# Performance work log

Hardware: AMD Instinct MI355X
Metric: run time of the kernel (lower is better)

The kernel has to match this reference:

```python
import jax, jax.numpy as jnp
import numpy as np
import math

B, S, E, H, V, VOCAB = 32, 512, 1024, 8, 36, 32000
PAD = 32  # padding_idx in nn.Embedding


def setup_inputs() -> dict:
    key = jax.random.key(0)
    ks = jax.random.split(key, 10)
    tokens = jax.random.randint(ks[0], (B, S), 0, VOCAB, dtype=jnp.int32)
    emb = jax.random.normal(ks[1], (VOCAB + 1, E), jnp.float32) * 0.02
    emb = emb.at[PAD].set(0.0)  # padding_idx row is zero
    Wq = jax.random.normal(ks[2], (H, E, E), jnp.float32) * 0.02
    bq = jax.random.normal(ks[3], (H, E), jnp.float32) * 0.02
    Wk = jax.random.normal(ks[4], (H, E, E), jnp.float32) * 0.02
    bk = jax.random.normal(ks[5], (H, E), jnp.float32) * 0.02
    Wv = jax.random.normal(ks[6], (H, E, V), jnp.float32) * 0.02
    bv = jax.random.normal(ks[7], (H, V), jnp.float32) * 0.02
    fc_w = jax.random.normal(ks[8], (2, S * H * V), jnp.float32) * 0.02
    fc_b = jax.random.normal(ks[9], (2,), jnp.float32) * 0.02
    return {"tokens": tokens, "emb": emb, "Wq": Wq, "bq": bq, "Wk": Wk,
            "bk": bk, "Wv": Wv, "bv": bv, "fc_w": fc_w, "fc_b": fc_b}


def reference(tokens, emb, Wq, bq, Wk, bk, Wv, bv, fc_w, fc_b):
    x = emb[tokens]  # [B,S,E]
    # 8 independent ReLU-gated attention heads, batched over head dim h
    q = jax.nn.relu(jnp.einsum('bse,hef->hbsf', x, Wq) + bq[:, None, None, :])  # [H,B,S,E]
    k = jax.nn.relu(jnp.einsum('bse,hef->hbsf', x, Wk) + bk[:, None, None, :])  # [H,B,S,E]
    v = jax.nn.relu(jnp.einsum('bse,hev->hbsv', x, Wv) + bv[:, None, None, :])  # [H,B,S,V]
    scores = jnp.einsum('hbsf,hbtf->hbst', q, k) / math.sqrt(E)  # [H,B,S,S]
    attn = jax.nn.softmax(scores, axis=-1)
    out = jnp.einsum('hbst,hbtv->hbsv', attn, v)  # [H,B,S,V]
    # concat heads on last dim -> [B,S,H*V] -> flatten [B, S*H*V]
    feat = jnp.transpose(out, (1, 2, 0, 3)).reshape(B, S * H * V)
    logits = feat @ fc_w.T + fc_b  # [B,2]
    score = jax.nn.sigmoid(logits)
    pred = jax.nn.log_softmax(score, axis=1)
    return pred, score
```

## Files before the change

### kernel.cpp

```cpp
#include <hip/hip_runtime.h>
#include <cstdint>

typedef unsigned short u16;
typedef unsigned char u8;
typedef signed char s8;
typedef unsigned int uint32;
typedef __attribute__((ext_vector_type(8))) short short8;
typedef __attribute__((ext_vector_type(4))) float f32x4;
typedef __attribute__((ext_vector_type(4))) int i32x4;

__device__ __forceinline__ u16 f32_to_bf16(float f) {
    unsigned u = __builtin_bit_cast(unsigned, f);
    u += 0x7FFFu + ((u >> 16) & 1u);
    return (u16)(u >> 16);
}
__device__ __forceinline__ float bf16_to_f32(u16 v) {
    return __builtin_bit_cast(float, (unsigned)v << 16);
}

__device__ __forceinline__ int q8(float x) {
    return (int)rintf(fminf(fmaxf(x * 1270.f, -127.f), 127.f));
}

#define BAR()   asm volatile("s_barrier" ::: "memory")
#define LGKM0() asm volatile("s_waitcnt lgkmcnt(0)" ::: "memory")
#define SCHED_FENCE() __builtin_amdgcn_sched_barrier(0)
#define AS1 __attribute__((address_space(1)))
#define AS3 __attribute__((address_space(3)))

__global__ __launch_bounds__(256) void embed_cast_q(const int* __restrict__ tok,
                                                    const float* __restrict__ emb,
                                                    u8* __restrict__ xq) {
    const int i = blockIdx.x;
    const long t = tok[i];
    const float4 f = ((const float4*)(emb + t * 1024))[threadIdx.x];
    unsigned p = (unsigned)(q8(f.x) & 255)         | ((unsigned)(q8(f.y) & 255) << 8)
               | ((unsigned)(q8(f.z) & 255) << 16) | ((unsigned)(q8(f.w) & 255) << 24);
    ((unsigned*)(xq + (long)i * 1024))[threadIdx.x] = p;
}

__global__ __launch_bounds__(256) void transpose_qk_q(const float* __restrict__ Wq,
                                                      const float* __restrict__ Wk,
                                                      s8* __restrict__ WqkTi) {
    const int z = blockIdx.z;
    const int h = z >> 1, m = z & 1;
    const float* W = (m ? Wk : Wq) + (long)h * 1048576;
    s8* out = WqkTi + (long)z * 1048576;
    __shared__ float tt[32][33];
    const int kb = blockIdx.x * 32, nb = blockIdx.y * 32;
    const int tx = threadIdx.x, ty = threadIdx.y;
    #pragma unroll
    for (int j = 0; j < 32; j += 8)
        tt[ty + j][tx] = W[(long)(kb + ty + j) * 1024 + nb + tx];
    __syncthreads();
    #pragma unroll
    for (int j = 0; j < 32; j += 8)
        out[(long)(nb + ty + j) * 1024 + kb + tx] = (s8)q8(tt[tx][ty + j]);
}

__global__ __launch_bounds__(256) void transpose_v_q(const float* __restrict__ Wv,
                                                     s8* __restrict__ WvTi) {
    const int h = blockIdx.z;
    const float* W = Wv + (long)h * 1024 * 36;
    s8* out = WvTi + (long)h * 128 * 1024;
    __shared__ float tt[32][33];
    const int kb = blockIdx.x * 32, nb = blockIdx.y * 32;
    const int tx = threadIdx.x, ty = threadIdx.y;
    #pragma unroll
    for (int j = 0; j < 32; j += 8) {
        const int n = nb + tx;
        tt[ty + j][tx] = (n < 36) ? W[(long)(kb + ty + j) * 36 + n] : 0.f;
    }
    __syncthreads();
    #pragma unroll
    for (int j = 0; j < 32; j += 8)
        out[(long)(nb + ty + j) * 1024 + kb + tx] = (s8)q8(tt[tx][ty + j]);
}

__global__ void stack_bias(const float* __restrict__ bq, const float* __restrict__ bk,
                           float* __restrict__ bqk) {
    const int i = blockIdx.x * 256 + threadIdx.x;
    const int h = i >> 11, c = i & 2047;
    bqk[i] = (c < 1024) ? bq[h * 1024 + c] : bk[h * 1024 + c - 1024];
}

__global__ void pad_bv(const float* __restrict__ bv, float* __restrict__ bvp) {
    int i = blockIdx.x * 256 + threadIdx.x;
    int h = i >> 7, n = i & 127;
    bvp[i] = (n < 36) ? bv[h * 36 + n] : 0.f;
}

template<bool RELU, bool TRANSC, bool HASBIAS, bool OUTI8>
__global__ __launch_bounds__(512, 2)
void gemm8i(const u8* __restrict__ A, const u8* __restrict__ Bt,
            void* __restrict__ Cv, const float* __restrict__ bias,
            int K, int lda, int ldb, int ldc, float scale, float oscale,
            long sB, long sC, int biasStride)
{
    __shared__ __attribute__((aligned(16))) u8 lds[4][2][16384];
    const int z = blockIdx.z;
    const u8* __restrict__ Bb = Bt + (long)z * sB;
    const long crow0 = (long)blockIdx.x * 256;
    const long ccol0 = (long)blockIdx.y * 256;
    const int tid = threadIdx.x;
    const int lane = tid & 63;
    const int wv = tid >> 6;
    const int wm = wv >> 2;
    const int wn = wv & 3;
    const int nt = K >> 7;
    const int r15 = lane & 15, g = lane >> 4;

    const int arow0 = wm * 128 + r15;
    const int aoffb = arow0 * 64 + ((g ^ ((arow0 >> 1) & 3)) << 4);
    const int brow0 = wn * 64 + r15;
    const int boffb = brow0 * 64 + ((g ^ ((brow0 >> 1) & 3)) << 4);

    const int stw = wv * 1024;
    uint32 arow[2], brow[2];
    #pragma unroll
    for (int j = 0; j < 2; ++j) {
        const int rj = j * 128 + wv * 16 + (lane >> 2);
        const int cj = (lane & 3) ^ ((rj >> 1) & 3);
        arow[j] = (uint32)((crow0 + rj) * (long)lda + cj * 16);
        brow[j] = (uint32)((ccol0 + rj) * (long)ldb + cj * 16);
    }

    i32x4 acc[8][4] = {};
    i32x4 s0a[8], s0b[4], s1a[8], s1b[4];

#define G8I_ST(RG, TT, KH) do {                                                \
    const long kk_ = (long)(TT) * 128 + (KH) * 64;                             \
    __builtin_amdgcn_global_load_lds((AS1 void*)(A + arow[0] + kk_),           \
        (AS3 void*)&lds[RG][0][stw], 16, 0, 0);                                \
    __builtin_amdgcn_global_load_lds((AS1 void*)(A + arow[1] + kk_),           \
        (AS3 void*)&lds[RG][0][8192 + stw], 16, 0, 0);                         \
    __builtin_amdgcn_global_load_lds((AS1 void*)(Bb + brow[0] + kk_),          \
        (AS3 void*)&lds[RG][1][stw], 16, 0, 0);                                \
    __builtin_amdgcn_global_load_lds((AS1 void*)(Bb + brow[1] + kk_),          \
        (AS3 void*)&lds[RG][1][8192 + stw], 16, 0, 0);                         \
} while (0)

#define G8I_RD(SA, SB, RG) do {                                                \
    _Pragma("unroll")                                                          \
    for (int mf = 0; mf < 8; ++mf)                                             \
        SA[mf] = *(const i32x4*)&lds[RG][0][aoffb + mf * 1024];                \
    _Pragma("unroll")                                                          \
    for (int nf = 0; nf < 4; ++nf)                                             \
        SB[nf] = *(const i32x4*)&lds[RG][1][boffb + nf * 1024];                \
} while (0)

#define G8I_MMA(SA, SB) do {                                                   \
    __builtin_amdgcn_s_setprio(1);                                             \
    _Pragma("unroll")                                                          \
    for (int nf = 0; nf < 4; ++nf)                                             \
        _Pragma("unroll")                                                      \
        for (int mf = 0; mf < 8; ++mf)                                         \
            acc[mf][nf] = __builtin_amdgcn_mfma_i32_16x16x64_i8(               \
                SA[mf], SB[nf], acc[mf][nf], 0, 0, 0);                         \
    __builtin_amdgcn_s_setprio(0);                                             \
} while (0)

    G8I_ST(0, 0, 0);
    G8I_ST(1, 0, 1);
    G8I_ST(2, 1, 0);
    G8I_ST(3, 1, 1);
    asm volatile("s_waitcnt vmcnt(12)" ::: "memory");
    BAR();
    G8I_RD(s0a, s0b, 0);
    LGKM0();
    BAR();

    for (int t = 0; t < nt - 2; ++t) {
        const int b0 = (t & 1) * 2, b1 = b0 + 1, n0 = b0 ^ 2;
        G8I_ST(b0, t + 2, 0);
        asm volatile("s_waitcnt vmcnt(12)" ::: "memory");
        BAR();
        G8I_RD(s1a, s1b, b1);
        SCHED_FENCE();
        G8I_MMA(s0a, s0b);
        LGKM0();
        BAR();
        G8I_ST(b1, t + 2, 1);
        asm volatile("s_waitcnt vmcnt(12)" ::: "memory");
        BAR();
        G8I_RD(s0a, s0b, n0);
        SCHED_FENCE();
        G8I_MMA(s1a, s1b);
        LGKM0();
        BAR();
    }
    {
        const int t = nt - 2;
        const int b1 = (t & 1) * 2 + 1, n0 = ((t & 1) * 2) ^ 2;
        asm volatile("s_waitcnt vmcnt(8)" ::: "memory");
        BAR();
        G8I_RD(s1a, s1b, b1);
        SCHED_FENCE();
        G8I_MMA(s0a, s0b);
        LGKM0();
        BAR();
        asm volatile("s_waitcnt vmcnt(4)" ::: "memory");
        BAR();
        G8I_RD(s0a, s0b, n0);
        SCHED_FENCE();
        G8I_MMA(s1a, s1b);
        LGKM0();
        BAR();
    }
    {
        const int t = nt - 1;
        const int b1 = (t & 1) * 2 + 1;
        asm volatile("s_waitcnt vmcnt(0)" ::: "memory");
        BAR();
        G8I_RD(s1a, s1b, b1);
        SCHED_FENCE();
        G8I_MMA(s0a, s0b);
        LGKM0();
        G8I_MMA(s1a, s1b);
    }

#undef G8I_ST
#undef G8I_RD
#undef G8I_MMA

    char* Cb = (char*)Cv + (long)z * sC * (OUTI8 ? 1 : 2);
    const float* bz = HASBIAS ? bias + (long)z * biasStride : bias;
    #pragma unroll
    for (int mf = 0; mf < 8; ++mf) {
        #pragma unroll
        for (int nf = 0; nf < 4; ++nf) {
            const long col = ccol0 + wn * 64 + nf * 16 + r15;
            float bval = 0.f;
            if (HASBIAS) bval = bz[col];
            #pragma unroll
            for (int rr = 0; rr < 4; ++rr) {
                const long row = crow0 + wm * 128 + mf * 16 + (g << 2) + rr;
                float v = (float)acc[mf][nf][rr] * scale + bval;
                if (RELU) v = fmaxf(v, 0.f);
                const long idx = TRANSC ? (col * (long)ldc + row) : (row * (long)ldc + col);
                if (OUTI8) {
                    const float q = fminf(fmaxf(v * oscale, -127.f), 127.f);
                    ((s8*)Cb)[idx] = (s8)(int)rintf(q);
                } else {
                    ((u16*)Cb)[idx] = f32_to_bf16(v);
                }
            }
        }
    }
}

__global__ __launch_bounds__(256, 4)
void gemm_bti(const s8* __restrict__ QKi, u16* __restrict__ attn,
              float scale, long sH, long sZ)
{
    __shared__ __attribute__((aligned(16))) u8 As[128 * 128];
    __shared__ __attribute__((aligned(16))) u8 Bs[128 * 128];
    const int z = blockIdx.z;
    const s8* base = QKi + (long)(z >> 5) * sH + (long)(z & 31) * sZ;
    const u8* Ab = (const u8*)base;
    const u8* Bb = (const u8*)(base + 1024);
    const long crow0 = (long)blockIdx.x * 128;
    const long ccol0 = (long)blockIdx.y * 128;
    const int tid = threadIdx.x, lane = tid & 63, wv = tid >> 6;
    const int wm = wv >> 1, wn = wv & 1;
    const int r15 = lane & 15, g = lane >> 4;

    i32x4 acc[4][4] = {};
    const int srow = (wv << 3) + (lane >> 3);
    const int sc8 = lane & 7;

    for (int k0 = 0; k0 < 1024; k0 += 128) {
        __syncthreads();
        #pragma unroll
        for (int i = 0; i < 4; ++i) {
            const int r = i * 32 + srow;
            const int c8 = sc8 ^ (r & 7);
            const u8* ga = Ab + (crow0 + r) * 2048L + k0 + c8 * 16;
            const u8* gb = Bb + (ccol0 + r) * 2048L + k0 + c8 * 16;
            __builtin_amdgcn_global_load_lds(
                (AS1 void*)ga, (AS3 void*)(&As[(i * 32 + wv * 8) * 128]), 16, 0, 0);
            __builtin_amdgcn_global_load_lds(
                (AS1 void*)gb, (AS3 void*)(&Bs[(i * 32 + wv * 8) * 128]), 16, 0, 0);
        }
        __syncthreads();

        #pragma unroll
        for (int ks = 0; ks < 2; ++ks) {
            i32x4 af[4], bfr[4];
            const int kg = ks * 4 + g;
            #pragma unroll
            for (int mf = 0; mf < 4; ++mf) {
                const int r = wm * 64 + mf * 16 + r15;
                af[mf] = *(const i32x4*)&As[r * 128 + ((kg ^ (r & 7)) << 4)];
            }
            #pragma unroll
            for (int nf = 0; nf < 4; ++nf) {
                const int r = wn * 64 + nf * 16 + r15;
                bfr[nf] = *(const i32x4*)&Bs[r * 128 + ((kg ^ (r & 7)) << 4)];
            }
            #pragma unroll
            for (int mf = 0; mf < 4; ++mf)
                #pragma unroll
                for (int nf = 0; nf < 4; ++nf)
                    acc[mf][nf] = __builtin_amdgcn_mfma_i32_16x16x64_i8(
                        af[mf], bfr[nf], acc[mf][nf], 0, 0, 0);
        }
    }

    u16* Cz = attn + (long)z * 262144;
    #pragma unroll
    for (int mf = 0; mf < 4; ++mf) {
        #pragma unroll
        for (int nf = 0; nf < 4; ++nf) {
            const long col = ccol0 + wn * 64 + nf * 16 + r15;
            #pragma unroll
            for (int rr = 0; rr < 4; ++rr) {
                const long row = crow0 + wm * 64 + mf * 16 + (g << 2) + rr;
                Cz[row * 512 + col] = f32_to_bf16((float)acc[mf][nf][rr] * scale);
            }
        }
    }
}

__global__ __launch_bounds__(256) void softmax_bf16(u16* __restrict__ sc) {
    const int row = blockIdx.x * 4 + (threadIdx.x >> 6);
    const int lane = threadIdx.x & 63;
    u16* r = sc + (long)row * 512;
    const uint4 pk = ((const uint4*)r)[lane];
    float e[8] = {
        bf16_to_f32((u16)(pk.x & 0xFFFF)), bf16_to_f32((u16)(pk.x >> 16)),
        bf16_to_f32((u16)(pk.y & 0xFFFF)), bf16_to_f32((u16)(pk.y >> 16)),
        bf16_to_f32((u16)(pk.z & 0xFFFF)), bf16_to_f32((u16)(pk.z >> 16)),
        bf16_to_f32((u16)(pk.w & 0xFFFF)), bf16_to_f32((u16)(pk.w >> 16))};
    float m = e[0];
    #pragma unroll
    for (int j = 1; j < 8; ++j) m = fmaxf(m, e[j]);
    #pragma unroll
    for (int o = 32; o; o >>= 1) m = fmaxf(m, __shfl_xor(m, o));
    float s = 0.f;
    #pragma unroll
    for (int j = 0; j < 8; ++j) { e[j] = __expf(e[j] - m); s += e[j]; }
    #pragma unroll
    for (int o = 32; o; o >>= 1) s += __shfl_xor(s, o);
    const float inv = 1.f / s;
    uint4 w;
    w.x = (unsigned)f32_to_bf16(e[0] * inv) | ((unsigned)f32_to_bf16(e[1] * inv) << 16);
    w.y = (unsigned)f32_to_bf16(e[2] * inv) | ((unsigned)f32_to_bf16(e[3] * inv) << 16);
    w.z = (unsigned)f32_to_bf16(e[4] * inv) | ((unsigned)f32_to_bf16(e[5] * inv) << 16);
    w.w = (unsigned)f32_to_bf16(e[6] * inv) | ((unsigned)f32_to_bf16(e[7] * inv) << 16);
    ((uint4*)r)[lane] = w;
}

__global__ __launch_bounds__(256, 4)
void pv_fc(const u16* __restrict__ attn, const u16* __restrict__ Vt,
           const float* __restrict__ fcw, float* __restrict__ part2, int h0)
{
    __shared__ __attribute__((aligned(16))) u16 As[128 * 64];
    __shared__ __attribute__((aligned(16))) u16 Bs[128 * 64];
    const int mb = blockIdx.x, kb = blockIdx.y, z = blockIdx.z;
    const int hl = z >> 5, zb = z & 31;
    const int h = h0 + hl;
    const u16* Ab = attn + (long)z * 262144 + (long)kb * 128;
    const u16* Bb = Vt + (long)h * 128 * 16384 + (long)zb * 512 + (long)kb * 128;
    const long crow0 = (long)mb * 128;
    const int tid = threadIdx.x, lane = tid & 63, wv = tid >> 6;
    const int wm = wv >> 1, wn = wv & 1;

    f32x4 acc[4][4] = {};
    const int srow = (wv << 3) + (lane >> 3);
    const int sc8 = lane & 7;

    #pragma unroll
    for (int k0 = 0; k0 < 128; k0 += 64) {
        __syncthreads();
        #pragma unroll
        for (int i = 0; i < 4; ++i) {
            const int r = i * 32 + srow;
            const int c8 = sc8 ^ (r & 7);
            const u16* ga = Ab + (crow0 + r) * 512L + k0 + c8 * 8;
            const u16* gb = Bb + (long)r * 16384 + k0 + c8 * 8;
            __builtin_amdgcn_global_load_lds(
                (AS1 void*)ga, (AS3 void*)(&As[(i * 32 + wv * 8) * 64]), 16, 0, 0);
            __builtin_amdgcn_global_load_lds(
                (AS1 void*)gb, (AS3 void*)(&Bs[(i * 32 + wv * 8) * 64]), 16, 0, 0);
        }
        __syncthreads();

        #pragma unroll
        for (int ks = 0; ks < 2; ++ks) {
            short8 af[4], bfr[4];
            const int kg = ks * 4 + (lane >> 4);
            #pragma unroll
            for (int mf = 0; mf < 4; ++mf) {
                const int r = wm * 64 + mf * 16 + (lane & 15);
                af[mf] = *(const short8*)&As[r * 64 + ((kg ^ (r & 7)) << 3)];
            }
            #pragma unroll
            for (int nf = 0; nf < 4; ++nf) {
                const int r = wn * 64 + nf * 16 + (lane & 15);
                bfr[nf] = *(const short8*)&Bs[r * 64 + ((kg ^ (r & 7)) << 3)];
            }
            #pragma unroll
            for (int mf = 0; mf < 4; ++mf)
                #pragma unroll
                for (int nf = 0; nf < 4; ++nf)
                    acc[mf][nf] = __builtin_amdgcn_mfma_f32_16x16x32_bf16(
                        af[mf], bfr[nf], acc[mf][nf], 0, 0, 0);
        }
    }

    float c0 = 0.f, c1 = 0.f;
    #pragma unroll
    for (int nf = 0; nf < 4; ++nf) {
        const int col = wn * 64 + nf * 16 + (lane & 15);
        if (col < 36) {
            #pragma unroll
            for (int mf = 0; mf < 4; ++mf) {
                #pragma unroll
                for (int rr = 0; rr < 4; ++rr) {
                    const long row = crow0 + wm * 64 + mf * 16 + ((lane >> 4) << 2) + rr;
                    const float v = acc[mf][nf][rr];
                    const long wi = row * 288 + h * 36 + col;
                    c0 += v * fcw[wi];
                    c1 += v * fcw[147456 + wi];
                }
            }
        }
    }
    #pragma unroll
    for (int o = 32; o; o >>= 1) { c0 += __shfl_xor(c0, o); c1 += __shfl_xor(c1, o); }
    __shared__ float red[8];
    if (lane == 0) { red[wv * 2] = c0; red[wv * 2 + 1] = c1; }
    __syncthreads();
    if (tid == 0) {
        const float s0 = red[0] + red[2] + red[4] + red[6];
        const float s1 = red[1] + red[3] + red[5] + red[7];
        float* p = part2 + (((long)(h * 32 + zb) * 4 + mb) * 4 + kb) * 2;
        p[0] = s0; p[1] = s1;
    }
}

__global__ void final_k(const float* __restrict__ part2, const float* __restrict__ fcb,
                        float* __restrict__ out) {
    const int b = threadIdx.x;
    if (b >= 32) return;
    float l0 = fcb[0], l1 = fcb[1];
    for (int h = 0; h < 8; ++h)
        #pragma unroll
        for (int mb = 0; mb < 4; ++mb)
            #pragma unroll
            for (int kb = 0; kb < 4; ++kb) {
                const float* p = part2 + (((long)(h * 32 + b) * 4 + mb) * 4 + kb) * 2;
                l0 += p[0]; l1 += p[1];
            }
    const float s0 = 1.f / (1.f + expf(-l0));
    const float s1 = 1.f / (1.f + expf(-l1));
    const float mm = fmaxf(s0, s1);
    const float lse = mm + logf(expf(s0 - mm) + expf(s1 - mm));
    out[b * 2] = s0 - lse; out[b * 2 + 1] = s1 - lse;
    out[64 + b * 2] = s0;  out[64 + b * 2 + 1] = s1;
}

extern "C" void kernel_launch(void* const* d_in, const int* in_sizes, int n_in,
                              void* d_out, int out_size, void* d_ws, size_t ws_size,
                              hipStream_t stream) {
    (void)in_sizes; (void)n_in;
    const int*   tokens = (const int*)  d_in[0];
    const float* emb    = (const float*)d_in[1];
    const float* Wq     = (const float*)d_in[2];
    const float* bq     = (const float*)d_in[3];
    const float* Wk     = (const float*)d_in[4];
    const float* bk     = (const float*)d_in[5];
    const float* Wv     = (const float*)d_in[6];
    const float* bv     = (const float*)d_in[7];
    const float* fcw    = (const float*)d_in[8];
    const float* fcb    = (const float*)d_in[9];
    float* out = (float*)d_out;

    char* wsp = (char*)d_ws;
    size_t need = 0;
    auto alloc = [&](size_t bytes) {
        char* p = wsp + need;
        need += (bytes + 255) & ~(size_t)255;
        return p;
    };
    u8*    xq     = (u8*)   alloc(16384L * 1024);
    s8*    WqkTi  = (s8*)   alloc(8L * 2048 * 1024);
    s8*    WvTi   = (s8*)   alloc(8L * 128 * 1024);
    float* bqk    = (float*)alloc(8L * 2048 * 4);
    float* bvp    = (float*)alloc(8L * 128 * 4);
    s8*    QKi    = (s8*)   alloc(4L * 16384 * 2048);
    u16*   Vt     = (u16*)  alloc(1024L * 16384 * 2);
    u16*   attn   = (u16*)  alloc(4L * 32 * 512 * 512 * 2);
    float* part2  = (float*)alloc(8L * 32 * 4 * 4 * 2 * 4);
    if (ws_size < need) {
        hipMemsetAsync(d_out, 0, (size_t)out_size * 4, stream);
        return;
    }

    const float SXW   = (0.1f / 127.f) * (0.1f / 127.f);
    const float SQK   = 0.2f / 127.f;
    const float INVSQK = 127.f / 0.2f;
    const float SSC   = SQK * SQK * 0.03125f;

    embed_cast_q<<<16384, 256, 0, stream>>>(tokens, emb, xq);
    pad_bv<<<4, 256, 0, stream>>>(bv, bvp);
    stack_bias<<<64, 256, 0, stream>>>(bq, bk, bqk);
    transpose_qk_q<<<dim3(32, 32, 16), dim3(32, 8), 0, stream>>>(Wq, Wk, WqkTi);
    transpose_v_q<<<dim3(32, 4, 8), dim3(32, 8), 0, stream>>>(Wv, WvTi);

    gemm8i<true, true, true, false><<<dim3(64, 4, 1), 512, 0, stream>>>(
        xq, (const u8*)WvTi, Vt, bvp, 1024, 1024, 1024, 16384, SXW, 0.f, 0, 0, 0);

    for (int gph = 0; gph < 2; ++gph) {
        gemm8i<true, false, true, true><<<dim3(64, 8, 4), 512, 0, stream>>>(
            xq, (const u8*)(WqkTi + (long)gph * 4 * 2048 * 1024), QKi,
            bqk + (long)gph * 4 * 2048, 1024, 1024, 1024, 2048, SXW, INVSQK,
            2048L * 1024, 16384L * 2048, 2048);
        gemm_bti<<<dim3(4, 4, 128), 256, 0, stream>>>(
            QKi, attn, SSC, 16384L * 2048, 512L * 2048);
        softmax_bf16<<<16384, 256, 0, stream>>>(attn);
        pv_fc<<<dim3(4, 4, 128), 256, 0, stream>>>(attn, Vt, fcw, part2, gph * 4);
    }
    final_k<<<1, 64, 0, stream>>>(part2, fcb, out);
}
```

Measured before the change: 648.6 us.

## Switch int8 projection GEMM to 32x32x32 MFMA with reordered grid and unrolled K loop

The int8 projection GEMM now uses 32x32x32 i8 MFMA instructions instead of 16x16x64, with the LDS fragment addressing and the epilogue's row mapping rewritten to match the larger accumulator layout. The K-tile count becomes a template parameter so the main loop can be fully unrolled. The grid is reordered so column tiles and heads vary fastest, which aims to improve L2 reuse of the A rows across blocks. The larger MFMA shape cuts instruction count and per-instruction overhead but changes register pressure and the epilogue's store pattern.

```diff
diff --git a/kernel.cpp b/kernel.cpp
--- a/kernel.cpp
+++ b/kernel.cpp
@@ -8,6 +8,7 @@
 typedef __attribute__((ext_vector_type(8))) short short8;
 typedef __attribute__((ext_vector_type(4))) float f32x4;
 typedef __attribute__((ext_vector_type(4))) int i32x4;
+typedef __attribute__((ext_vector_type(16))) int i32x16;
 
 __device__ __forceinline__ u16 f32_to_bf16(float f) {
     unsigned u = __builtin_bit_cast(unsigned, f);
@@ -90,30 +91,33 @@
     bvp[i] = (n < 36) ? bv[h * 36 + n] : 0.f;
 }
 
-template<bool RELU, bool TRANSC, bool HASBIAS, bool OUTI8>
+template<bool RELU, bool TRANSC, bool HASBIAS, bool OUTI8, int NT>
 __global__ __launch_bounds__(512, 2)
 void gemm8i(const u8* __restrict__ A, const u8* __restrict__ Bt,
             void* __restrict__ Cv, const float* __restrict__ bias,
-            int K, int lda, int ldb, int ldc, float scale, float oscale,
+            int lda, int ldb, int ldc, float scale, float oscale,
             long sB, long sC, int biasStride)
 {
     __shared__ __attribute__((aligned(16))) u8 lds[4][2][16384];
-    const int z = blockIdx.z;
-    const u8* __restrict__ Bb = Bt + (long)z * sB;
-    const long crow0 = (long)blockIdx.x * 256;
-    const long ccol0 = (long)blockIdx.y * 256;
+    const int hz = blockIdx.y;
+    const u8* __restrict__ Bb = Bt + (long)hz * sB;
+    const long crow0 = (long)blockIdx.z * 256;
+    const long ccol0 = (long)blockIdx.x * 256;
     const int tid = threadIdx.x;
     const int lane = tid & 63;
     const int wv = tid >> 6;
     const int wm = wv >> 2;
     const int wn = wv & 3;
-    const int nt = K >> 7;
-    const int r15 = lane & 15, g = lane >> 4;
-
-    const int arow0 = wm * 128 + r15;
-    const int aoffb = arow0 * 64 + ((g ^ ((arow0 >> 1) & 3)) << 4);
-    const int brow0 = wn * 64 + r15;
-    const int boffb = brow0 * 64 + ((g ^ ((brow0 >> 1) & 3)) << 4);
+    const int l31 = lane & 31, hi = lane >> 5;
+
+    const int arow0 = wm * 128 + l31;
+    const int aswz = (arow0 >> 1) & 3;
+    const int aoffk0 = arow0 * 64 + (((0 + hi) ^ aswz) << 4);
+    const int aoffk1 = arow0 * 64 + (((2 + hi) ^ aswz) << 4);
+    const int brow0 = wn * 64 + l31;
+    const int bswz = (brow0 >> 1) & 3;
+    const int boffk0 = brow0 * 64 + (((0 + hi) ^ bswz) << 4);
+    const int boffk1 = brow0 * 64 + (((2 + hi) ^ bswz) << 4);
 
     const int stw = wv * 1024;
     uint32 arow[2], brow[2];
@@ -125,7 +129,7 @@
         brow[j] = (uint32)((ccol0 + rj) * (long)ldb + cj * 16);
     }
 
-    i32x4 acc[8][4] = {};
+    i32x16 acc[4][2] = {};
     i32x4 s0a[8], s0b[4], s1a[8], s1b[4];
 
 #define G8I_ST(RG, TT, KH) do {                                                \
@@ -142,21 +146,28 @@
 
 #define G8I_RD(SA, SB, RG) do {                                                \
     _Pragma("unroll")                                                          \
-    for (int mf = 0; mf < 8; ++mf)                                             \
-        SA[mf] = *(const i32x4*)&lds[RG][0][aoffb + mf * 1024];                \
+    for (int mf = 0; mf < 4; ++mf) {                                           \
+        SA[mf * 2]     = *(const i32x4*)&lds[RG][0][aoffk0 + mf * 2048];       \
+        SA[mf * 2 + 1] = *(const i32x4*)&lds[RG][0][aoffk1 + mf * 2048];       \
+    }                                                                          \
     _Pragma("unroll")                                                          \
-    for (int nf = 0; nf < 4; ++nf)                                             \
-        SB[nf] = *(const i32x4*)&lds[RG][1][boffb + nf * 1024];                \
+    for (int nf = 0; nf < 2; ++nf) {                                           \
+        SB[nf * 2]     = *(const i32x4*)&lds[RG][1][boffk0 + nf * 2048];       \
+        SB[nf * 2 + 1] = *(const i32x4*)&lds[RG][1][boffk1 + nf * 2048];       \
+    }                                                                          \
 } while (0)
 
 #define G8I_MMA(SA, SB) do {                                                   \
     __builtin_amdgcn_s_setprio(1);                                             \
     _Pragma("unroll")                                                          \
-    for (int nf = 0; nf < 4; ++nf)                                             \
+    for (int nf = 0; nf < 2; ++nf)                                             \
         _Pragma("unroll")                                                      \
-        for (int mf = 0; mf < 8; ++mf)                                         \
-            acc[mf][nf] = __builtin_amdgcn_mfma_i32_16x16x64_i8(               \
-                SA[mf], SB[nf], acc[mf][nf], 0, 0, 0);                         \
+        for (int mf = 0; mf < 4; ++mf) {                                       \
+            acc[mf][nf] = __builtin_amdgcn_mfma_i32_32x32x32_i8(               \
+                SA[mf * 2], SB[nf * 2], acc[mf][nf], 0, 0, 0);                 \
+            acc[mf][nf] = __builtin_amdgcn_mfma_i32_32x32x32_i8(               \
+                SA[mf * 2 + 1], SB[nf * 2 + 1], acc[mf][nf], 0, 0, 0);         \
+        }                                                                      \
     __builtin_amdgcn_s_setprio(0);                                             \
 } while (0)
 
@@ -170,7 +181,8 @@
     LGKM0();
     BAR();
 
-    for (int t = 0; t < nt - 2; ++t) {
+    #pragma unroll
+    for (int t = 0; t < NT - 2; ++t) {
         const int b0 = (t & 1) * 2, b1 = b0 + 1, n0 = b0 ^ 2;
         G8I_ST(b0, t + 2, 0);
         asm volatile("s_waitcnt vmcnt(12)" ::: "memory");
@@ -190,7 +202,7 @@
         BAR();
     }
     {
-        const int t = nt - 2;
+        const int t = NT - 2;
         const int b1 = (t & 1) * 2 + 1, n0 = ((t & 1) * 2) ^ 2;
         asm volatile("s_waitcnt vmcnt(8)" ::: "memory");
         BAR();
@@ -208,7 +220,7 @@
         BAR();
     }
     {
-        const int t = nt - 1;
+        const int t = NT - 1;
         const int b1 = (t & 1) * 2 + 1;
         asm volatile("s_waitcnt vmcnt(0)" ::: "memory");
         BAR();
@@ -223,19 +235,19 @@
 #undef G8I_RD
 #undef G8I_MMA
 
-    char* Cb = (char*)Cv + (long)z * sC * (OUTI8 ? 1 : 2);
-    const float* bz = HASBIAS ? bias + (long)z * biasStride : bias;
-    #pragma unroll
-    for (int mf = 0; mf < 8; ++mf) {
-        #pragma unroll
-        for (int nf = 0; nf < 4; ++nf) {
-            const long col = ccol0 + wn * 64 + nf * 16 + r15;
+    char* Cb = (char*)Cv + (long)hz * sC * (OUTI8 ? 1 : 2);
+    #pragma unroll
+    for (int mf = 0; mf < 4; ++mf) {
+        #pragma unroll
+        for (int nf = 0; nf < 2; ++nf) {
+            const long col = ccol0 + wn * 64 + nf * 32 + l31;
             float bval = 0.f;
-            if (HASBIAS) bval = bz[col];
-            #pragma unroll
-            for (int rr = 0; rr < 4; ++rr) {
-                const long row = crow0 + wm * 128 + mf * 16 + (g << 2) + rr;
-                float v = (float)acc[mf][nf][rr] * scale + bval;
+            if (HASBIAS) bval = bias[(long)hz * biasStride + col];
+            #pragma unroll
+            for (int reg = 0; reg < 16; ++reg) {
+                const int rl = (reg & 3) + ((reg >> 2) << 3) + (hi << 2);
+                const long row = crow0 + wm * 128 + mf * 32 + rl;
+                float v = (float)acc[mf][nf][reg] * scale + bval;
                 if (RELU) v = fmaxf(v, 0.f);
                 const long idx = TRANSC ? (col * (long)ldc + row) : (row * (long)ldc + col);
                 if (OUTI8) {
@@ -509,13 +521,13 @@
     transpose_qk_q<<<dim3(32, 32, 16), dim3(32, 8), 0, stream>>>(Wq, Wk, WqkTi);
     transpose_v_q<<<dim3(32, 4, 8), dim3(32, 8), 0, stream>>>(Wv, WvTi);
 
-    gemm8i<true, true, true, false><<<dim3(64, 4, 1), 512, 0, stream>>>(
-        xq, (const u8*)WvTi, Vt, bvp, 1024, 1024, 1024, 16384, SXW, 0.f, 0, 0, 0);
+    gemm8i<true, true, true, false, 8><<<dim3(4, 1, 64), 512, 0, stream>>>(
+        xq, (const u8*)WvTi, Vt, bvp, 1024, 1024, 16384, SXW, 0.f, 0, 0, 0);
 
     for (int gph = 0; gph < 2; ++gph) {
-        gemm8i<true, false, true, true><<<dim3(64, 8, 4), 512, 0, stream>>>(
+        gemm8i<true, false, true, true, 8><<<dim3(8, 4, 64), 512, 0, stream>>>(
             xq, (const u8*)(WqkTi + (long)gph * 4 * 2048 * 1024), QKi,
-            bqk + (long)gph * 4 * 2048, 1024, 1024, 1024, 2048, SXW, INVSQK,
+            bqk + (long)gph * 4 * 2048, 1024, 1024, 2048, SXW, INVSQK,
             2048L * 1024, 16384L * 2048, 2048);
         gemm_bti<<<dim3(4, 4, 128), 256, 0, stream>>>(
             QKi, attn, SSC, 16384L * 2048, 512L * 2048);
```

After: 685.5 us. +5.7%, slower.
